# Optimization experiments

Hardware: AMD Instinct MI355X
Metric: run time of the kernel (lower is better)

Reference implementation:

```python
import jax, jax.numpy as jnp
import numpy as np


def setup_inputs() -> dict:
    key = jax.random.key(0)
    k1, k2 = jax.random.split(key)
    N = 8192
    # Inputs are lower-triangular by contract of the original module.
    A = jnp.tril(jax.random.normal(k1, (N, N), dtype=jnp.float32))
    B = jnp.tril(jax.random.normal(k2, (N, N), dtype=jnp.float32))
    return {"A": A, "B": B}


def reference(A, B):
    # C = tril(A @ B): product of two lower-triangular matrices is lower
    # triangular; the original applies tril to zero numerical garbage in the
    # strictly-upper part (and to enforce it in the fallback path).
    return jnp.tril(jnp.matmul(A, B))
```

## Files before the change

kernel.cpp:

```cpp
#include <hip/hip_runtime.h>
#include <hip/hip_bf16.h>
#include <type_traits>
#include <utility>


static constexpr int MATN = 8192;

typedef __attribute__((ext_vector_type(8))) short  s8v;
typedef __attribute__((ext_vector_type(4))) short  s4h;
typedef __attribute__((ext_vector_type(8))) __bf16 b8v;
typedef __attribute__((ext_vector_type(4))) float  f4v;

template <typename V, typename = void>
struct mfma_ok : std::false_type {};
template <typename V>
struct mfma_ok<V, std::void_t<decltype(__builtin_amdgcn_mfma_f32_16x16x32_bf16(
    std::declval<V>(), std::declval<V>(), std::declval<f4v>(), 0, 0, 0))>>
    : std::true_type {};
using abv = std::conditional_t<mfma_ok<b8v>::value, b8v, s8v>;

__device__ __forceinline__ short f2bf(float f) {
  unsigned u = __builtin_bit_cast(unsigned, f);
  unsigned r = (u + 0x7fffu + ((u >> 16) & 1u)) >> 16;
  return (short)r;
}

__device__ __forceinline__ void async16(void* lds, const void* g) {
  __builtin_amdgcn_global_load_lds(
      (const __attribute__((address_space(1))) unsigned int*)g,
      (__attribute__((address_space(3))) unsigned int*)lds, 16, 0, 0);
}

__device__ __forceinline__ int tri_decode(int id) {
  int k = (int)((sqrtf(8.0f * (float)id + 1.0f) - 1.0f) * 0.5f);
  while ((k + 1) * (k + 2) / 2 <= id) k++;
  while (k * (k + 1) / 2 > id) k--;
  return k;
}

__global__ __launch_bounds__(256) void convert_A_k(const float* __restrict__ A,
                                                   short* __restrict__ Abf) {
  int gid  = blockIdx.x * 256 + threadIdx.x;
  int base = gid * 8;
  int row  = base >> 13;
  int col  = base & 8191;
  s8v o = {};
  if (col <= row) {
    f4v v0 = *(const f4v*)&A[base];
    f4v v1 = *(const f4v*)&A[base + 4];
#pragma unroll
    for (int i = 0; i < 4; i++) { o[i] = f2bf(v0[i]); o[4 + i] = f2bf(v1[i]); }
  }
  *(s8v*)&Abf[base] = o;
}

__global__ __launch_bounds__(256) void transpose_B_k(const float* __restrict__ B,
                                                     short* __restrict__ Bt) {
  __shared__ __align__(16) short T[64 * 68];
  int k0 = blockIdx.x * 64, n0 = blockIdx.y * 64;
  int tid = threadIdx.x;
  if (k0 + 63 < n0) {
    s8v z = {};
#pragma unroll
    for (int t = 0; t < 2; t++) {
      int c = t * 256 + tid;
      int n = c >> 3, kg = c & 7;
      *(s8v*)&Bt[(size_t)(n0 + n) * MATN + k0 + kg * 8] = z;
    }
    return;
  }
#pragma unroll
  for (int t = 0; t < 4; t++) {
    int c = t * 256 + tid;
    int k = c >> 4, cn = c & 15;
    s4h o = {};
    if (n0 + cn * 4 <= k0 + k) {
      f4v v = *(const f4v*)&B[(size_t)(k0 + k) * MATN + n0 + cn * 4];
#pragma unroll
      for (int i = 0; i < 4; i++) o[i] = f2bf(v[i]);
    }
    int cs = cn ^ (2 * (k >> 3));
    *(s4h*)&T[k * 68 + cs * 4] = o;
  }
  __syncthreads();
#pragma unroll
  for (int t = 0; t < 2; t++) {
    int c = t * 256 + tid;
    int n = c >> 3, kg = c & 7;
    int nn = n ^ (kg * 8);
    s8v o;
#pragma unroll
    for (int i = 0; i < 8; i++) o[i] = T[(kg * 8 + i) * 68 + nn];
    *(s8v*)&Bt[(size_t)(n0 + n) * MATN + k0 + kg * 8] = o;
  }
}

__global__ __launch_bounds__(256) void gemm_tril(const short* __restrict__ Abf,
                                                 const short* __restrict__ Btb,
                                                 float* __restrict__ C) {
  int id = blockIdx.x;
  int tid = threadIdx.x;
  int bi, bj;
  if (id < 2304) {
    int s = id >> 6;
    int t = tri_decode(s);
    int J = s - t * (t + 1) / 2;
    int I = J + 7 - t;
    int li = 7 - ((id >> 3) & 7);
    int lj = id & 7;
    bi = I * 8 + li;
    bj = J * 8 + lj;
  } else {
    int q = id - 2304;
    int s = q >> 6;
    int r = tri_decode(s);
    int I = s - r * (r + 1) / 2;
    int J = r + 1;
    bi = I * 8 + ((q >> 3) & 7);
    bj = J * 8 + (q & 7);
  }

  if (bi < bj) {
    f4v z = {};
    size_t base = (size_t)bi * 128 * MATN + (size_t)bj * 128;
#pragma unroll
    for (int t = 0; t < 16; t++) {
      int c = t * 256 + tid;
      int r2 = c >> 5, cc = (c & 31) * 4;
      *(f4v*)&C[base + (size_t)r2 * MATN + cc] = z;
    }
    return;
  }

  __shared__ __align__(16) short As[128 * 32];
  __shared__ __align__(16) short Bs[128 * 32];

  int wave = tid >> 6, lane = tid & 63;
  int quad = lane >> 4, ln = lane & 15;
  int wm = wave >> 1, wn = wave & 1;

  int row0 = bi * 128, col0 = bj * 128;
  f4v acc[4][4] = {};

  int r0 = tid >> 2, c0 = (tid & 3) * 8;
  int r1 = 64 + r0;
  char* lA0 = (char*)As + wave * 1024;
  char* lA1 = (char*)As + 4096 + wave * 1024;
  char* lB0 = (char*)Bs + wave * 1024;
  char* lB1 = (char*)Bs + 4096 + wave * 1024;

  int kend = (bi + 1) * 128;
  for (int kt = col0; kt < kend; kt += 32) {
    __syncthreads();
    async16(lA0, &Abf[(size_t)(row0 + r0) * MATN + kt + c0]);
    async16(lA1, &Abf[(size_t)(row0 + r1) * MATN + kt + c0]);
    async16(lB0, &Btb[(size_t)(col0 + r0) * MATN + kt + c0]);
    async16(lB1, &Btb[(size_t)(col0 + r1) * MATN + kt + c0]);
    __syncthreads();

    abv a[4], b[4];
#pragma unroll
    for (int t = 0; t < 4; t++) {
      a[t] = *(const abv*)&As[(wm * 64 + t * 16 + ln) * 32 + quad * 8];
      b[t] = *(const abv*)&Bs[(wn * 64 + t * 16 + ln) * 32 + quad * 8];
    }
#pragma unroll
    for (int tm = 0; tm < 4; tm++)
#pragma unroll
      for (int tn = 0; tn < 4; tn++)
        acc[tm][tn] = __builtin_amdgcn_mfma_f32_16x16x32_bf16(
            a[tm], b[tn], acc[tm][tn], 0, 0, 0);
  }

  bool diag = (bi == bj);
#pragma unroll
  for (int tm = 0; tm < 4; tm++) {
    int grb = row0 + wm * 64 + tm * 16 + quad * 4;
#pragma unroll
    for (int tn = 0; tn < 4; tn++) {
      int gc = col0 + wn * 64 + tn * 16 + ln;
#pragma unroll
      for (int r = 0; r < 4; r++) {
        int gr = grb + r;
        float v = acc[tm][tn][r];
        if (diag && gr < gc) v = 0.0f;
        C[(size_t)gr * MATN + gc] = v;
      }
    }
  }
}

__global__ __launch_bounds__(256) void gemm_tril_f32(const float* __restrict__ A,
                                                     const float* __restrict__ B,
                                                     float* __restrict__ C) {
  int bj = blockIdx.x, bi = blockIdx.y;
  int tid = threadIdx.x;
  int row0 = bi * 64, col0 = bj * 64;
  if (bi < bj) {
    f4v z = {};
#pragma unroll
    for (int t = 0; t < 4; t++) {
      int c = t * 256 + tid;
      int r = c >> 4, cc = (c & 15) * 4;
      *(f4v*)&C[(size_t)(row0 + r) * MATN + col0 + cc] = z;
    }
    return;
  }
  __shared__ float As[64][17];
  __shared__ float Bs[16][65];
  int tx = tid & 15, ty = tid >> 4;
  float acc[4][4] = {};
  int kendf = (bi + 1) * 64;
  for (int kt = col0; kt < kendf; kt += 16) {
    __syncthreads();
#pragma unroll
    for (int t = 0; t < 4; t++) {
      int c = t * 256 + tid;
      int r = c >> 4, k = c & 15;
      As[r][k] = A[(size_t)(row0 + r) * MATN + kt + k];
    }
#pragma unroll
    for (int t = 0; t < 4; t++) {
      int c = t * 256 + tid;
      int k = c >> 6, n = c & 63;
      Bs[k][n] = B[(size_t)(kt + k) * MATN + col0 + n];
    }
    __syncthreads();
#pragma unroll
    for (int k = 0; k < 16; k++) {
      float av[4], bv[4];
#pragma unroll
      for (int i = 0; i < 4; i++) av[i] = As[ty * 4 + i][k];
#pragma unroll
      for (int j = 0; j < 4; j++) bv[j] = Bs[k][tx * 4 + j];
#pragma unroll
      for (int i = 0; i < 4; i++)
#pragma unroll
        for (int j = 0; j < 4; j++) acc[i][j] += av[i] * bv[j];
    }
  }
#pragma unroll
  for (int i = 0; i < 4; i++)
#pragma unroll
    for (int j = 0; j < 4; j++) {
      int gr = row0 + ty * 4 + i, gc = col0 + tx * 4 + j;
      C[(size_t)gr * MATN + gc] = (gr >= gc) ? acc[i][j] : 0.0f;
    }
}

extern "C" void kernel_launch(void* const* d_in, const int* in_sizes, int n_in,
                              void* d_out, int out_size, void* d_ws, size_t ws_size,
                              hipStream_t stream) {
  const float* A = (const float*)d_in[0];
  const float* B = (const float*)d_in[1];
  float* C = (float*)d_out;

  const size_t need = 2ull * MATN * MATN * sizeof(short);
  if (ws_size >= need) {
    short* Abf = (short*)d_ws;
    short* Btb = Abf + (size_t)MATN * MATN;
    convert_A_k<<<(MATN * (size_t)MATN) / 8 / 256, 256, 0, stream>>>(A, Abf);
    transpose_B_k<<<dim3(MATN / 64, MATN / 64), 256, 0, stream>>>(B, Btb);
    gemm_tril<<<4096, 256, 0, stream>>>(Abf, Btb, C);
  } else {
    gemm_tril_f32<<<dim3(MATN / 64, MATN / 64), 256, 0, stream>>>(A, B, C);
  }
}
```

Before: 900.7 us.

## Transpose B via identity MFMA and stage GEMM output through LDS

```diff
diff --git a/kernel.cpp b/kernel.cpp
--- a/kernel.cpp
+++ b/kernel.cpp
@@ -23,6 +23,12 @@
   unsigned u = __builtin_bit_cast(unsigned, f);
   unsigned r = (u + 0x7fffu + ((u >> 16) & 1u)) >> 16;
   return (short)r;
+}
+
+template <typename V>
+__device__ __forceinline__ void set_bits(V& v, int i, short bits) {
+  if constexpr (std::is_same_v<V, s8v>) v[i] = bits;
+  else v[i] = __builtin_bit_cast(__bf16, bits);
 }
 
 __device__ __forceinline__ void async16(void* lds, const void* g) {
@@ -54,45 +60,45 @@
   *(s8v*)&Abf[base] = o;
 }
 
-__global__ __launch_bounds__(256) void transpose_B_k(const float* __restrict__ B,
-                                                     short* __restrict__ Bt) {
-  __shared__ __align__(16) short T[64 * 68];
-  int k0 = blockIdx.x * 64, n0 = blockIdx.y * 64;
+__global__ __launch_bounds__(256) void mfma_transpose_B(const float* __restrict__ B,
+                                                        short* __restrict__ Bt) {
+  int kb = blockIdx.x, nb = blockIdx.y;
+  int K0 = kb * 64, n0 = nb * 32;
   int tid = threadIdx.x;
-  if (k0 + 63 < n0) {
+  if (K0 + 63 < n0) {
+    int row = tid >> 3, ch = tid & 7;
     s8v z = {};
-#pragma unroll
-    for (int t = 0; t < 2; t++) {
-      int c = t * 256 + tid;
-      int n = c >> 3, kg = c & 7;
-      *(s8v*)&Bt[(size_t)(n0 + n) * MATN + k0 + kg * 8] = z;
-    }
+    *(s8v*)&Bt[(size_t)(n0 + row) * MATN + K0 + ch * 8] = z;
     return;
   }
-#pragma unroll
-  for (int t = 0; t < 4; t++) {
-    int c = t * 256 + tid;
-    int k = c >> 4, cn = c & 15;
-    s4h o = {};
-    if (n0 + cn * 4 <= k0 + k) {
-      f4v v = *(const f4v*)&B[(size_t)(k0 + k) * MATN + n0 + cn * 4];
-#pragma unroll
-      for (int i = 0; i < 4; i++) o[i] = f2bf(v[i]);
-    }
-    int cs = cn ^ (2 * (k >> 3));
-    *(s4h*)&T[k * 68 + cs * 4] = o;
-  }
-  __syncthreads();
-#pragma unroll
-  for (int t = 0; t < 2; t++) {
-    int c = t * 256 + tid;
-    int n = c >> 3, kg = c & 7;
-    int nn = n ^ (kg * 8);
-    s8v o;
-#pragma unroll
-    for (int i = 0; i < 8; i++) o[i] = T[(kg * 8 + i) * 68 + nn];
-    *(s8v*)&Bt[(size_t)(n0 + n) * MATN + k0 + kg * 8] = o;
-  }
+  int wave = tid >> 6, lane = tid & 63;
+  int quad = lane >> 4, ln = lane & 15;
+  int k0w = K0 + wave * 16;
+
+  const float* src = &B[(size_t)(k0w + ln) * MATN + n0 + quad * 8];
+  f4v v0 = *(const f4v*)src;
+  f4v v1 = *(const f4v*)(src + 4);
+  abv af;
+#pragma unroll
+  for (int i = 0; i < 4; i++) {
+    set_bits(af, i,     f2bf(v0[i]));
+    set_bits(af, 4 + i, f2bf(v1[i]));
+  }
+  abv I0, I1;
+#pragma unroll
+  for (int j = 0; j < 8; j++) {
+    set_bits(I0, j, (short)((8 * quad + j == ln)      ? 0x3F80 : 0));
+    set_bits(I1, j, (short)((8 * quad + j == ln + 16) ? 0x3F80 : 0));
+  }
+  f4v d0 = {}, d1 = {};
+  d0 = __builtin_amdgcn_mfma_f32_16x16x32_bf16(af, I0, d0, 0, 0, 0);
+  d1 = __builtin_amdgcn_mfma_f32_16x16x32_bf16(af, I1, d1, 0, 0, 0);
+
+  s4h o0, o1;
+#pragma unroll
+  for (int r = 0; r < 4; r++) { o0[r] = f2bf(d0[r]); o1[r] = f2bf(d1[r]); }
+  *(s4h*)&Bt[(size_t)(n0 + ln) * MATN + k0w + quad * 4]      = o0;
+  *(s4h*)&Bt[(size_t)(n0 + 16 + ln) * MATN + k0w + quad * 4] = o1;
 }
 
 __global__ __launch_bounds__(256) void gemm_tril(const short* __restrict__ Abf,
@@ -132,8 +138,9 @@
     return;
   }
 
-  __shared__ __align__(16) short As[128 * 32];
-  __shared__ __align__(16) short Bs[128 * 32];
+  __shared__ __align__(16) char smem[16384];
+  short* As = (short*)smem;
+  short* Bs = (short*)(smem + 8192);
 
   int wave = tid >> 6, lane = tid & 63;
   int quad = lane >> 4, ln = lane & 15;
@@ -173,19 +180,30 @@
   }
 
   bool diag = (bi == bj);
+  float* Ct = (float*)smem;
 #pragma unroll
   for (int tm = 0; tm < 4; tm++) {
-    int grb = row0 + wm * 64 + tm * 16 + quad * 4;
+    __syncthreads();
 #pragma unroll
     for (int tn = 0; tn < 4; tn++) {
-      int gc = col0 + wn * 64 + tn * 16 + ln;
+      int col = wn * 64 + tn * 16 + ln;
+      int gc = col0 + col;
 #pragma unroll
       for (int r = 0; r < 4; r++) {
-        int gr = grb + r;
+        int lrow = wm * 16 + quad * 4 + r;
+        int gr = row0 + wm * 64 + tm * 16 + quad * 4 + r;
         float v = acc[tm][tn][r];
         if (diag && gr < gc) v = 0.0f;
-        C[(size_t)gr * MATN + gc] = v;
+        Ct[lrow * 128 + col] = v;
       }
+    }
+    __syncthreads();
+#pragma unroll
+    for (int w = 0; w < 4; w++) {
+      int chunk = w * 256 + tid;
+      int lrow = chunk >> 5, c4 = (chunk & 31) * 4;
+      int gr = row0 + (lrow >> 4) * 64 + tm * 16 + (lrow & 15);
+      *(f4v*)&C[(size_t)gr * MATN + col0 + c4] = *(const f4v*)&Ct[lrow * 128 + c4];
     }
   }
 }
@@ -260,7 +278,7 @@
     short* Abf = (short*)d_ws;
     short* Btb = Abf + (size_t)MATN * MATN;
     convert_A_k<<<(MATN * (size_t)MATN) / 8 / 256, 256, 0, stream>>>(A, Abf);
-    transpose_B_k<<<dim3(MATN / 64, MATN / 64), 256, 0, stream>>>(B, Btb);
+    mfma_transpose_B<<<dim3(MATN / 64, MATN / 32), 256, 0, stream>>>(B, Btb);
     gemm_tril<<<4096, 256, 0, stream>>>(Abf, Btb, C);
   } else {
     gemm_tril_f32<<<dim3(MATN / 64, MATN / 64), 256, 0, stream>>>(A, B, C);
```

New measurement: 921.9 us. 2.4% more time.
